# Performance work log

Hardware: AMD Instinct MI355X
Metric: run time of the kernel (lower is better)

The kernel has to match this reference:

```python
import jax, jax.numpy as jnp
import numpy as np

H = 128; D_T = 512; D_C = 256
NT = 20000; NC = 100000
E_TC = 100000; E_SIM = 800000; E_TS = 640000
K_APPNP = 10; ALPHA = 0.2


def setup_inputs() -> dict:
    key = jax.random.key(0)
    ki = iter(jax.random.split(key, 64))
    def nrm(shape, scale=1.0):
        return jax.random.normal(next(ki), shape, jnp.float32) * scale
    inp = {
        'table_x': nrm((NT, D_T)),
        'column_x': nrm((NC, D_C)),
        'q': nrm((D_T,)),
    }
    # layer-1 SAGEConv params per edge type: (src_dim, dst_dim)
    dims1 = {'tc': (D_T, D_C), 'rev': (D_C, D_T), 'cs': (D_C, D_C),
             'ns': (D_C, D_C), 'ds': (D_C, D_C), 'ts': (D_T, D_T)}
    for et, (dsrc, ddst) in dims1.items():
        inp['Wl1_' + et] = nrm((dsrc, H), 1.0 / np.sqrt(dsrc))
        inp['bl1_' + et] = jnp.zeros((H,), jnp.float32)
        inp['Wr1_' + et] = nrm((ddst, H), 1.0 / np.sqrt(ddst))
    # layer-2: only the convs that feed the 'table' output are needed
    for et in ('rev', 'ts'):
        inp['Wl2_' + et] = nrm((H, H), 1.0 / np.sqrt(H))
        inp['bl2_' + et] = jnp.zeros((H,), jnp.float32)
        inp['Wr2_' + et] = nrm((H, H), 1.0 / np.sqrt(H))
    inp['Wq'] = nrm((D_T, H), 1.0 / np.sqrt(D_T))
    inp['bq'] = jnp.zeros((H,), jnp.float32)
    inp['Wlin'] = nrm((H, 1), 1.0 / np.sqrt(H))
    inp['blin'] = jnp.zeros((1,), jnp.float32)
    inp['ts_ew'] = jax.random.uniform(next(ki), (E_TS,), jnp.float32)
    inp['tc_src'] = jax.random.randint(next(ki), (E_TC,), 0, NT)
    inp['tc_dst'] = jax.random.randint(next(ki), (E_TC,), 0, NC)
    inp['cs_ei'] = jax.random.randint(next(ki), (2, E_SIM), 0, NC)
    inp['ns_ei'] = jax.random.randint(next(ki), (2, E_SIM), 0, NC)
    inp['ds_ei'] = jax.random.randint(next(ki), (2, E_SIM), 0, NC)
    inp['ts_ei'] = jax.random.randint(next(ki), (2, E_TS), 0, NT)
    return inp


def _sage(xs, xd, src, dst, Wl, bl, Wr, n_dst):
    # PyG SAGEConv: lin_l(mean_{j in N(i)} x_j) + lin_r(x_i).
    # Linear commutes with mean, so project src features first (cheap gather).
    m = (xs @ Wl)[src]                                     # [E, H]
    s = jax.ops.segment_sum(m, dst, num_segments=n_dst)    # [n_dst, H]
    c = jax.ops.segment_sum(jnp.ones(src.shape, m.dtype), dst, num_segments=n_dst)
    return s / jnp.maximum(c, 1.0)[:, None] + bl + xd @ Wr


def _appnp(x, src, dst, ew, n):
    # gcn_norm with self-loops (fill value 1), then K personalized-PageRank steps
    loop = jnp.arange(n)
    s2 = jnp.concatenate([src, loop])
    d2 = jnp.concatenate([dst, loop])
    w2 = jnp.concatenate([ew, jnp.ones((n,), x.dtype)])
    deg = jax.ops.segment_sum(w2, d2, num_segments=n)
    dis = jnp.where(deg > 0, 1.0 / jnp.sqrt(deg), 0.0)
    norm = dis[s2] * w2 * dis[d2]                           # [E+n]
    def step(z, _):
        h = jax.ops.segment_sum(norm[:, None] * z[s2], d2, num_segments=n)
        return (1.0 - ALPHA) * h + ALPHA * x, None
    z, _ = jax.lax.scan(step, x, None, length=K_APPNP)
    return z


def reference(table_x, column_x, q, Wl1_tc, bl1_tc, Wr1_tc, Wl1_rev, bl1_rev, Wr1_rev,
              Wl1_cs, bl1_cs, Wr1_cs, Wl1_ns, bl1_ns, Wr1_ns, Wl1_ds, bl1_ds, Wr1_ds,
              Wl1_ts, bl1_ts, Wr1_ts, Wl2_rev, bl2_rev, Wr2_rev, Wl2_ts, bl2_ts, Wr2_ts,
              Wq, bq, Wlin, blin, ts_ew, tc_src, tc_dst, cs_ei, ns_ei, ds_ei, ts_ei):
    nT, nC = table_x.shape[0], column_x.shape[0]
    # ---- HeteroConv layer 1 (sum over edge types per destination type) ----
    col1 = (_sage(table_x, column_x, tc_src, tc_dst, Wl1_tc, bl1_tc, Wr1_tc, nC)
            + _sage(column_x, column_x, cs_ei[0], cs_ei[1], Wl1_cs, bl1_cs, Wr1_cs, nC)
            + _sage(column_x, column_x, ns_ei[0], ns_ei[1], Wl1_ns, bl1_ns, Wr1_ns, nC)
            + _sage(column_x, column_x, ds_ei[0], ds_ei[1], Wl1_ds, bl1_ds, Wr1_ds, nC))
    tab1 = (_sage(column_x, table_x, tc_dst, tc_src, Wl1_rev, bl1_rev, Wr1_rev, nT)
            + _sage(table_x, table_x, ts_ei[0], ts_ei[1], Wl1_ts, bl1_ts, Wr1_ts, nT))
    col1 = jax.nn.relu(col1)
    tab1 = jax.nn.relu(tab1)
    # ---- HeteroConv layer 2 (only the 'table' output is consumed) ----
    tab2 = (_sage(col1, tab1, tc_dst, tc_src, Wl2_rev, bl2_rev, Wr2_rev, nT)
            + _sage(tab1, tab1, ts_ei[0], ts_ei[1], Wl2_ts, bl2_ts, Wr2_ts, nT))
    # ---- retrieval-weighted query injection ----
    qv = q @ Wq + bq                                        # [H]
    eps = 1e-12
    xr = table_x / jnp.maximum(jnp.linalg.norm(table_x, axis=1, keepdims=True), eps)
    qr = q / jnp.maximum(jnp.linalg.norm(q), eps)
    wgt = jnp.maximum(xr @ qr, 0.0)                         # [nT]
    z0 = wgt[:, None] * qv[None, :]                         # [nT, H]
    # ---- APPNP diffusion over the table-sim graph ----
    z = _appnp(tab2 + z0, ts_ei[0], ts_ei[1], ts_ew, nT)
    return (z @ Wlin + blin)[:, 0]
```

## Files before the change

kernel.cpp:

```cpp
#include <hip/hip_runtime.h>

#define NT 20000
#define NC 100000
#define DT 512
#define DC 256
#define E_TC 100000
#define E_SIM 800000
#define E_TS 640000

#define KB_COL 0
#define KB_TAB (4 * NC)
#define NKEY   (4 * NC + 2 * NT)
#define NED_AB (3 * E_SIM + E_TC + E_TC + E_TS)
#define COLSTR 112
#define TABSTR 96
#define NPASS  4

typedef float f32x4 __attribute__((ext_vector_type(4)));
typedef __bf16 bf16x8 __attribute__((ext_vector_type(8)));


struct WD { const float* w0; const float* w1; const float* w2; const float* w3;
            __bf16* out; int K; int kshift; int ebase; };
struct WD8 { WD d[8]; };

__global__ void wprep_all(WD8 ds, int total) {
    int i = blockIdx.x * blockDim.x + threadIdx.x;
    if (i >= total) return;
#pragma unroll
    for (int s = 7; s >= 0; --s) {
        if (i >= ds.d[s].ebase) {
            const WD d = ds.d[s];
            const int idx = i - d.ebase;
            const int n = idx >> d.kshift;
            const int k = idx & (d.K - 1);
            float v = d.w0[(size_t)k * 128 + n];
            if (d.w1) v += d.w1[(size_t)k * 128 + n];
            if (d.w2) v += d.w2[(size_t)k * 128 + n];
            if (d.w3) v += d.w3[(size_t)k * 128 + n];
            d.out[(size_t)n * d.K + k] = (__bf16)v;
            return;
        }
    }
}

__global__ void vecprep(const float* __restrict__ q, const float* __restrict__ Wq,
                        const float* __restrict__ bq,
                        const float* __restrict__ Wr2_rev, const float* __restrict__ Wr2_ts,
                        const float* __restrict__ Wl2_rev, const float* __restrict__ Wl2_ts,
// ... 10 lines not shown
    biasT1[t] = bl1_rev[t] + bl1_ts[t];
    float a = 0.f, b = 0.f, c = 0.f;
    for (int h = 0; h < 128; ++h) {
        const float wl = Wlin[h];
        a = fmaf(Wr2_rev[(size_t)t * 128 + h] + Wr2_ts[(size_t)t * 128 + h], wl, a);
        b = fmaf(Wl2_rev[(size_t)t * 128 + h], wl, b);
        c = fmaf(Wl2_ts[(size_t)t * 128 + h], wl, c);
    }
    w2s[t] = a; wrev[t] = b; wts[t] = c;
    float qv = bq[t];
    for (int k = 0; k < 512; ++k) qv = fmaf(q[k], Wq[(size_t)k * 128 + t], qv);
    __shared__ float sh[128];
    sh[t] = qv * Wlin[t];
    __syncthreads();
    for (int st = 64; st >= 1; st >>= 1) { if (t < st) sh[t] += sh[t + st]; __syncthreads(); }
    if (t == 0) sc[0] = sh[0];
    __syncthreads();
    sh[t] = (bl2_rev[t] + bl2_ts[t]) * Wlin[t];
    __syncthreads();
    for (int st = 64; st >= 1; st >>= 1) { if (t < st) sh[t] += sh[t + st]; __syncthreads(); }
    if (t == 0) sc[1] = sh[0];
    __syncthreads();
    float ss = 0.f;
    for (int k = t; k < 512; k += 128) { const float v = q[k]; ss = fmaf(v, v, ss); }
    sh[t] = ss;
    __syncthreads();
    for (int st = 64; st >= 1; st >>= 1) { if (t < st) sh[t] += sh[t + st]; __syncthreads(); }
    if (t == 0) sc[2] = fmaxf(sqrtf(sh[0]), 1e-12f);
}


struct B5 { const __bf16* p[5]; };
struct Y5 { __bf16* p[5]; };

__launch_bounds__(256, 2)
__global__ void gemm_col5(const float* __restrict__ X, B5 wp, const float* __restrict__ bias,
                          Y5 yp, int M) {
    __shared__ __bf16 Bs[128 * 256];
    const int t = threadIdx.x;
    const int lane = t & 63;
    const int wave = t >> 6;
    const int l15 = lane & 15;
    const int kg = lane >> 4;
    const int rowbase = blockIdx.x * 128 + wave * 32;

    bf16x8 af[2][8];
#pragma unroll
    for (int m = 0; m < 2; ++m) {
        int r = rowbase + m * 16 + l15;
        r = (r < M) ? r : (M - 1);
        const float* baseA = X + (size_t)r * 256 + kg * 8;
#pragma unroll
        for (int ks = 0; ks < 8; ++ks) {
            const float4 x0 = *reinterpret_cast<const float4*>(baseA + ks * 32);
            const float4 x1 = *reinterpret_cast<const float4*>(baseA + ks * 32 + 4);
            bf16x8 tt;
            tt[0] = (__bf16)x0.x; tt[1] = (__bf16)x0.y; tt[2] = (__bf16)x0.z; tt[3] = (__bf16)x0.w;
            tt[4] = (__bf16)x1.x; tt[5] = (__bf16)x1.y; tt[6] = (__bf16)x1.z; tt[7] = (__bf16)x1.w;
            af[m][ks] = tt;
        }
    }

#pragma unroll
    for (int o = 0; o < 5; ++o) {
        __syncthreads();
        const __bf16* Wt = wp.p[o];
#pragma unroll
        for (int i = 0; i < 16; ++i) {
            const int u = t + i * 256;
            const int row = u >> 5;
            const int ku = u & 31;
            const bf16x8 v = *reinterpret_cast<const bf16x8*>(Wt + (size_t)row * 256 + ku * 8);
            *reinterpret_cast<bf16x8*>(&Bs[row * 256 + ((ku ^ (row & 7)) << 3)]) = v;
        }
        __syncthreads();
        f32x4 acc[2][8];
#pragma unroll
        for (int m = 0; m < 2; ++m)
#pragma unroll
            for (int n = 0; n < 8; ++n) acc[m][n] = (f32x4)0.f;
#pragma unroll
        for (int ks = 0; ks < 8; ++ks) {
            const int ku = ks * 4 + kg;
#pragma unroll
            for (int n = 0; n < 8; ++n) {
                const int r = n * 16 + l15;
                const bf16x8 bf = *reinterpret_cast<const bf16x8*>(&Bs[r * 256 + ((ku ^ (r & 7)) << 3)]);
                acc[0][n] = __builtin_amdgcn_mfma_f32_16x16x32_bf16(af[0][ks], bf, acc[0][n], 0, 0, 0);
                acc[1][n] = __builtin_amdgcn_mfma_f32_16x16x32_bf16(af[1][ks], bf, acc[1][n], 0, 0, 0);
            }
        }
        __bf16* Y = yp.p[o];
#pragma unroll
        for (int n = 0; n < 8; ++n) {
            const int col = n * 16 + l15;
            const float bv = (o == 0) ? bias[col] : 0.f;
#pragma unroll
            for (int m = 0; m < 2; ++m)
#pragma unroll
                for (int rr = 0; rr < 4; ++rr) {
                    const int row = rowbase + m * 16 + kg * 4 + rr;
                    if (row < M) Y[(size_t)row * 128 + col] = (__bf16)(acc[m][n][rr] + bv);
                }
        }
    }
}

struct B3 { const __bf16* p[3]; };
struct Y3 { __bf16* p[3]; };

__launch_bounds__(256, 2)
__global__ void gemm_tab3(const float* __restrict__ X, B3 wp, const float* __restrict__ bias,
                          Y3 yp, const float* __restrict__ q, const float* __restrict__ sc,
                          float* __restrict__ wgt, int M) {
    __shared__ __bf16 Bs[128 * 256];
    const int t = threadIdx.x;
    const int lane = t & 63;
    const int wave = t >> 6;
    const int l15 = lane & 15;
    const int kg = lane >> 4;
    const int rowbase = blockIdx.x * 64 + wave * 16;
    const int r0 = rowbase + l15;
    const bool rv = r0 < M;
    const int rc = rv ? r0 : (M - 1);
    const float* baseA = X + (size_t)rc * 512 + kg * 8;

    bf16x8 af[16];
    float dot = 0.f, ss = 0.f;
#pragma unroll
    for (int ks = 0; ks < 16; ++ks) {
        const float4 x0 = *reinterpret_cast<const float4*>(baseA + ks * 32);
        const float4 x1 = *reinterpret_cast<const float4*>(baseA + ks * 32 + 4);
        const float4 q0 = *reinterpret_cast<const float4*>(q + kg * 8 + ks * 32);
        const float4 q1 = *reinterpret_cast<const float4*>(q + kg * 8 + ks * 32 + 4);
        dot += x0.x * q0.x + x0.y * q0.y + x0.z * q0.z + x0.w * q0.w
             + x1.x * q1.x + x1.y * q1.y + x1.z * q1.z + x1.w * q1.w;
        ss += x0.x * x0.x + x0.y * x0.y + x0.z * x0.z + x0.w * x0.w
            + x1.x * x1.x + x1.y * x1.y + x1.z * x1.z + x1.w * x1.w;
        bf16x8 tt;
        tt[0] = (__bf16)x0.x; tt[1] = (__bf16)x0.y; tt[2] = (__bf16)x0.z; tt[3] = (__bf16)x0.w;
        tt[4] = (__bf16)x1.x; tt[5] = (__bf16)x1.y; tt[6] = (__bf16)x1.z; tt[7] = (__bf16)x1.w;
        af[ks] = tt;
    }
    dot += __shfl_xor(dot, 16); dot += __shfl_xor(dot, 32);
    ss  += __shfl_xor(ss, 16);  ss  += __shfl_xor(ss, 32);
    if (lane < 16 && rv) {
        const float nx = fmaxf(sqrtf(ss), 1e-12f);
        wgt[r0] = fmaxf(dot, 0.f) / (nx * sc[2]);
    }

#pragma unroll
    for (int o = 0; o < 3; ++o) {
        f32x4 acc[8];
#pragma unroll
        for (int n = 0; n < 8; ++n) acc[n] = (f32x4)0.f;
        const __bf16* Wt = wp.p[o];
#pragma unroll
        for (int c = 0; c < 2; ++c) {
            __syncthreads();
#pragma unroll
            for (int i = 0; i < 16; ++i) {
                const int u = t + i * 256;
                const int row = u >> 5;
                const int ku = u & 31;
                const bf16x8 v = *reinterpret_cast<const bf16x8*>(Wt + (size_t)row * 512 + c * 256 + ku * 8);
                *reinterpret_cast<bf16x8*>(&Bs[row * 256 + ((ku ^ (row & 7)) << 3)]) = v;
            }
            __syncthreads();
#pragma unroll
            for (int ks = 0; ks < 8; ++ks) {
                const int ku = ks * 4 + kg;
#pragma unroll
                for (int n = 0; n < 8; ++n) {
                    const int r = n * 16 + l15;
                    const bf16x8 bf = *reinterpret_cast<const bf16x8*>(&Bs[r * 256 + ((ku ^ (r & 7)) << 3)]);
                    acc[n] = __builtin_amdgcn_mfma_f32_16x16x32_bf16(af[c * 8 + ks], bf, acc[n], 0, 0, 0);
                }
            }
        }
        __bf16* Y = yp.p[o];
#pragma unroll
        for (int n = 0; n < 8; ++n) {
            const int col = n * 16 + l15;
            const float bv = (o == 0) ? bias[col] : 0.f;
#pragma unroll
            for (int rr = 0; rr < 4; ++rr) {
                const int row = rowbase + kg * 4 + rr;
                if (row < M) Y[(size_t)row * 128 + col] = (__bf16)(acc[n][rr] + bv);
            }
        }
    }
}


struct ED { const int* dst; const int* src; int E; int ebase; int ng; int g;
            int keybase; int srcoff; int ts; };
struct ED6 { ED d[6]; };

__global__ void fill_win(ED6 ds, const float* __restrict__ ew_ts,
                         const float* __restrict__ dis, int* __restrict__ cur,
                         int* __restrict__ ed_idx, int2* __restrict__ edT,
                         int lo, int hi, int total) {
    int e = blockIdx.x * blockDim.x + threadIdx.x;
    if (e >= total) return;
#pragma unroll
    for (int i = 5; i >= 0; --i) {
        if (e >= ds.d[i].ebase) {
            const ED d = ds.d[i];
            const int le = e - d.ebase;
            const int dstv = d.dst[le];
            const int key = d.keybase + dstv * d.ng + d.g;
            if (key >= lo && key < hi) {
                const int srcv = d.src[le];
                const int slot = atomicAdd(&cur[key], 1);
                if (key < KB_TAB) {
                    const int g = key & 3;
                    const int cap = (g < 3) ? 32 : 16;
                    if (slot < cap)
                        ed_idx[(key >> 2) * COLSTR + g * 32 + slot] = d.srcoff + srcv;
                } else {
                    const int k2 = key - KB_TAB;
                    const int g = k2 & 1;
                    const int cap = g ? 72 : 24;
                    if (slot < cap) {
                        int2 v;
                        v.x = d.srcoff + srcv;
                        v.y = d.ts ? __float_as_int(dis[srcv] * ew_ts[le] * dis[dstv]) : 0;
                        edT[(k2 >> 1) * TABSTR + g * 24 + slot] = v;
                    }
                }
            }
            return;
        }
    }
}

__global__ void deg_accum(const int* __restrict__ dst, const float* __restrict__ ew,
                          float* __restrict__ deg, int E) {
    int e = blockIdx.x * blockDim.x + threadIdx.x;
    if (e < E) atomicAdd(&deg[dst[e]], ew[e]);
}

__global__ void deg_to_dis(float* __restrict__ deg, int n) {
    int i = blockIdx.x * blockDim.x + threadIdx.x;
    if (i < n) {
        float d = deg[i];
        deg[i] = (d > 0.f) ? (1.0f / sqrtf(d)) : 0.f;
    }
}

__global__ void fill_f32(float* __restrict__ p, float v, int n) {
    int i = blockIdx.x * blockDim.x + threadIdx.x;
    if (i < n) p[i] = v;
}


__launch_bounds__(256)
__global__ void col_fused(const __bf16* __restrict__ selfRow, const __bf16* __restrict__ featCat,
                          const int* __restrict__ cur, const int* __restrict__ ed_idx,
                          const float* __restrict__ wvec, float* __restrict__ outv, int n) {
    const int wave = threadIdx.x >> 6;
    const int lane = threadIdx.x & 63;
    const int sg = lane >> 4;
    const int sl = lane & 15;
    const int row = blockIdx.x * 4 + wave;
    if (row >= n) return;
    const int4 l4 = *reinterpret_cast<const int4*>(&cur[row * 4]);
    int len[4];
    len[0] = (l4.x < 32) ? l4.x : 32;
    len[1] = (l4.y < 32) ? l4.y : 32;
    len[2] = (l4.z < 32) ? l4.z : 32;
    len[3] = (l4.w < 16) ? l4.w : 16;
    const int rowbase = row * COLSTR;
    float s8[8] = {0.f, 0.f, 0.f, 0.f, 0.f, 0.f, 0.f, 0.f};
#pragma unroll
    for (int g = 0; g < 4; ++g) {
        const int lg = len[g];
        if (lg <= 0) continue;
        const int base = rowbase + g * 32;
        const float w = 1.0f / (float)lg;
        int j = sg;
        for (; j + 4 < lg; j += 8) {
            const int s0 = ed_idx[base + j];
            const int s1 = ed_idx[base + j + 4];
            const bf16x8 v0 = *reinterpret_cast<const bf16x8*>(&featCat[(size_t)s0 * 128 + sl * 8]);
            const bf16x8 v1 = *reinterpret_cast<const bf16x8*>(&featCat[(size_t)s1 * 128 + sl * 8]);
// ... 65 lines not shown
        if (j < lg) {
            const int s0 = edT[base + j].x;
            const bf16x8 v0 = *reinterpret_cast<const bf16x8*>(&featCat[(size_t)s0 * 128 + sl * 8]);
#pragma unroll
            for (int t = 0; t < 8; ++t) s8[t] = fmaf(w, (float)v0[t], s8[t]);
        }
    }
#pragma unroll
    for (int t = 0; t < 8; ++t) {
        s8[t] += __shfl_xor(s8[t], 16);
        s8[t] += __shfl_xor(s8[t], 32);
    }
    const bf16x8 gv = *reinterpret_cast<const bf16x8*>(&selfRow[(size_t)row * 128 + sl * 8]);
    const float4 a0 = *reinterpret_cast<const float4*>(&wa[sl * 8]);
    const float4 a1 = *reinterpret_cast<const float4*>(&wa[sl * 8 + 4]);
    const float4 b0 = *reinterpret_cast<const float4*>(&wb[sl * 8]);
    const float4 b1 = *reinterpret_cast<const float4*>(&wb[sl * 8 + 4]);
    const float wwa[8] = {a0.x, a0.y, a0.z, a0.w, a1.x, a1.y, a1.z, a1.w};
    const float wwb[8] = {b0.x, b0.y, b0.z, b0.w, b1.x, b1.y, b1.z, b1.w};
    float da = 0.f, db = 0.f;
#pragma unroll
    for (int t = 0; t < 8; ++t) {
        const float rv = fmaxf(s8[t] + (float)gv[t], 0.f);
        da = fmaf(rv, wwa[t], da);
        db = fmaf(rv, wwb[t], db);
    }
#pragma unroll
    for (int off = 8; off; off >>= 1) { da += __shfl_xor(da, off); db += __shfl_xor(db, off); }
    if (lane == 0) { ya[row] = da; yb[row] = db; }
}


__launch_bounds__(256)
__global__ void y0_joint(const float* __restrict__ tvs, const float* __restrict__ val2,
                         const int* __restrict__ cur, const int2* __restrict__ edT,
                         const float* __restrict__ wgt, const float* __restrict__ sc,
                         float* __restrict__ y0, int n) {
    const int row = blockIdx.x * 16 + (threadIdx.x >> 4);
    const int l = threadIdx.x & 15;
    if (row >= n) return;
    const int2 l2 = *reinterpret_cast<const int2*>(&cur[KB_TAB + row * 2]);
    int len[2];
    len[0] = (l2.x < 24) ? l2.x : 24;
    len[1] = (l2.y < 72) ? l2.y : 72;
    const int rowbase = row * TABSTR;
    float s = 0.f;
#pragma unroll
    for (int g = 0; g < 2; ++g) {
        const int lg = len[g];
        if (lg <= 0) continue;
        const int base = rowbase + g * 24;
        const float w = 1.0f / (float)lg;
        for (int j = l; j < lg; j += 16)
            s = fmaf(w, val2[edT[base + j].x], s);
    }
#pragma unroll
    for (int off = 8; off; off >>= 1) s += __shfl_xor(s, off);
    if (l == 0) y0[row] = tvs[row] + sc[1] + wgt[row] * sc[0] + s;
}

__launch_bounds__(256)
__global__ void appnp_s(const float* __restrict__ z, const float* __restrict__ y0,
                        const int* __restrict__ cur, const int2* __restrict__ edT,
                        const float* __restrict__ dis, float* __restrict__ zo,
                        const float* __restrict__ blin, float* __restrict__ out,
                        int n, int last) {
    const int row = blockIdx.x * 16 + (threadIdx.x >> 4);
    const int l = threadIdx.x & 15;
    if (row >= n) return;
    int lg = cur[KB_TAB + row * 2 + 1];
    lg = (lg < 72) ? lg : 72;
    const int base = row * TABSTR + 24;
    float s = 0.f;
    int j = l;
    for (; j + 16 < lg; j += 32) {
        const int2 p0 = edT[base + j];
        const int2 p1 = edT[base + j + 16];
        s = fmaf(__int_as_float(p0.y), z[p0.x - NC], s);
        s = fmaf(__int_as_float(p1.y), z[p1.x - NC], s);
    }
    if (j < lg) {
        const int2 p0 = edT[base + j];
        s = fmaf(__int_as_float(p0.y), z[p0.x - NC], s);
    }
#pragma unroll
    for (int off = 8; off; off >>= 1) s += __shfl_xor(s, off);
    if (l == 0) {
        const float d = dis[row];
        const float v = 0.8f * (s + d * d * z[row]) + 0.2f * y0[row];
        if (last) out[row] = v + blin[0];
        else zo[row] = v;
    }
}


extern "C" void kernel_launch(void* const* d_in, const int* in_sizes, int n_in,
                              void* d_out, int out_size, void* d_ws, size_t ws_size,
                              hipStream_t stream) {
    const float* table_x  = (const float*)d_in[0];
    const float* column_x = (const float*)d_in[1];
    const float* q        = (const float*)d_in[2];
    const float* Wl1_tc  = (const float*)d_in[3];  const float* bl1_tc  = (const float*)d_in[4];  const float* Wr1_tc  = (const float*)d_in[5];
    const float* Wl1_rev = (const float*)d_in[6];  const float* bl1_rev = (const float*)d_in[7];  const float* Wr1_rev = (const float*)d_in[8];
    const float* Wl1_cs  = (const float*)d_in[9];  const float* bl1_cs  = (const float*)d_in[10]; const float* Wr1_cs  = (const float*)d_in[11];
    const float* Wl1_ns  = (const float*)d_in[12]; const float* bl1_ns  = (const float*)d_in[13]; const float* Wr1_ns  = (const float*)d_in[14];
    const float* Wl1_ds  = (const float*)d_in[15]; const float* bl1_ds  = (const float*)d_in[16]; const float* Wr1_ds  = (const float*)d_in[17];
    const float* Wl1_ts  = (const float*)d_in[18]; const float* bl1_ts  = (const float*)d_in[19]; const float* Wr1_ts  = (const float*)d_in[20];
    const float* Wl2_rev = (const float*)d_in[21]; const float* bl2_rev = (const float*)d_in[22]; const float* Wr2_rev = (const float*)d_in[23];
    const float* Wl2_ts  = (const float*)d_in[24]; const float* bl2_ts  = (const float*)d_in[25]; const float* Wr2_ts  = (const float*)d_in[26];
    const float* Wq   = (const float*)d_in[27]; const float* bq   = (const float*)d_in[28];
    const float* Wlin = (const float*)d_in[29]; const float* blin = (const float*)d_in[30];
    const float* ts_ew = (const float*)d_in[31];
    const int* tc_src = (const int*)d_in[32];
    const int* tc_dst = (const int*)d_in[33];
    const int* cs_ei  = (const int*)d_in[34];
    const int* ns_ei  = (const int*)d_in[35];
    const int* ds_ei  = (const int*)d_in[36];
    const int* ts_ei  = (const int*)d_in[37];

    char* w = (char*)d_ws;
    size_t off = 0;
    auto alloc = [&](size_t bytes) -> void* {
        void* p = w + off;
        off += (bytes + 255) & ~(size_t)255;
// ... 32 lines not shown
    float* f_wrev = (float*)alloc(128 * 4);
    float* f_wts  = (float*)alloc(128 * 4);
    float* f_sc   = (float*)alloc(16 * 4);
    int* i_cur  = (int*)alloc((size_t)NKEY * 4);
    int* ed_idx = (int*)alloc((size_t)NC * COLSTR * 4);
    int2* edT   = (int2*)alloc((size_t)NT * TABSTR * 8);
    if (off > ws_size) return;

    auto cdiv = [](int a, int b) { return (a + b - 1) / b; };

    {
        WD8 ds;
        int eb = 0;
        auto set = [&](int i, const float* a, const float* b2, const float* c, const float* d2,
                       __bf16* o, int K, int ksh) {
            ds.d[i] = {a, b2, c, d2, o, K, ksh, eb};
            eb += 128 * K;
        };
        set(0, Wr1_tc, Wr1_cs, Wr1_ns, Wr1_ds, WtS1c, 256, 8);
        set(1, Wl1_cs, nullptr, nullptr, nullptr, Wt_cs, 256, 8);
        set(2, Wl1_ns, nullptr, nullptr, nullptr, Wt_ns, 256, 8);
        set(3, Wl1_ds, nullptr, nullptr, nullptr, Wt_ds, 256, 8);
        set(4, Wl1_rev, nullptr, nullptr, nullptr, Wt_rev, 256, 8);
        set(5, Wl1_tc, nullptr, nullptr, nullptr, Wt_tc, 512, 9);
        set(6, Wr1_rev, Wr1_ts, nullptr, nullptr, WtS1t, 512, 9);
        set(7, Wl1_ts, nullptr, nullptr, nullptr, Wt_ts, 512, 9);
        wprep_all<<<cdiv(eb, 256), 256, 0, stream>>>(ds, eb);
    }
    vecprep<<<1, 128, 0, stream>>>(q, Wq, bq, Wr2_rev, Wr2_ts, Wl2_rev, Wl2_ts,
                                   bl2_rev, bl2_ts, Wlin, bl1_tc, bl1_cs, bl1_ns, bl1_ds,
                                   bl1_rev, bl1_ts, f_biasC, f_biasT1,
                                   f_w2s, f_wrev, f_wts, f_sc);

    {
        B5 wp; wp.p[0] = WtS1c; wp.p[1] = Wt_cs; wp.p[2] = Wt_ns; wp.p[3] = Wt_ds; wp.p[4] = Wt_rev;
        Y5 yp; yp.p[0] = gemmC; yp.p[1] = projC_cs; yp.p[2] = projC_ns; yp.p[3] = projC_ds; yp.p[4] = projC_rev;
        gemm_col5<<<cdiv(NC, 128), 256, 0, stream>>>(column_x, wp, f_biasC, yp, NC);
    }
    {
        B3 wp; wp.p[0] = WtS1t; wp.p[1] = Wt_tc; wp.p[2] = Wt_ts;
        Y3 yp; yp.p[0] = gemmT; yp.p[1] = projT_tc; yp.p[2] = projT_ts;
        gemm_tab3<<<cdiv(NT, 64), 256, 0, stream>>>(table_x, wp, f_biasT1, yp, q, f_sc, f_wgt, NT);
    }

    ED6 cds;
    cds.d[0] = {cs_ei + E_SIM, cs_ei, E_SIM, 0,                  4, 0, KB_COL, 0,      0};
    cds.d[1] = {ns_ei + E_SIM, ns_ei, E_SIM, E_SIM,              4, 1, KB_COL, NC,     0};
    cds.d[2] = {ds_ei + E_SIM, ds_ei, E_SIM, 2 * E_SIM,          4, 2, KB_COL, 2 * NC, 0};
    cds.d[3] = {tc_dst, tc_src, E_TC, 3 * E_SIM,                 4, 3, KB_COL, 3 * NC, 0};
    cds.d[4] = {tc_src, tc_dst, E_TC, 3 * E_SIM + E_TC,          2, 0, KB_TAB, 0,      0};
    cds.d[5] = {ts_ei + E_TS, ts_ei, E_TS, 3 * E_SIM + 2 * E_TC, 2, 1, KB_TAB, NC,     1};

    fill_f32<<<cdiv(NT, 256), 256, 0, stream>>>(f_dis, 1.0f, NT);
    deg_accum<<<cdiv(E_TS, 256), 256, 0, stream>>>(ts_ei + E_TS, ts_ew, f_dis, E_TS);
    deg_to_dis<<<cdiv(NT, 256), 256, 0, stream>>>(f_dis, NT);
    hipMemsetAsync(i_cur, 0, (size_t)NKEY * 4, stream);
    for (int p = 0; p < NPASS; ++p) {
        const int lo = (int)((long long)NKEY * p / NPASS);
        const int hi = (int)((long long)NKEY * (p + 1) / NPASS);
        fill_win<<<cdiv(NED_AB, 256), 256, 0, stream>>>(cds, ts_ew, f_dis, i_cur,
                                                        ed_idx, edT, lo, hi, NED_AB);
    }

    col_fused<<<cdiv(NC, 4), 256, 0, stream>>>(gemmC, featC, i_cur, ed_idx,
                                               f_wrev, f_colv, NC);
    tab_fused<<<cdiv(NT, 4), 256, 0, stream>>>(gemmT, featT, i_cur, edT,
                                               f_w2s, f_wts, f_tvs, f_tvt, NT);

    y0_joint<<<cdiv(NT, 16), 256, 0, stream>>>(f_tvs, val2, i_cur, edT,
                                               f_wgt, f_sc, f_y0, NT);

    const float* zin = f_y0;
    float* zout = f_za;
    for (int it = 0; it < 10; ++it) {
        const int last = (it == 9);
        appnp_s<<<cdiv(NT, 16), 256, 0, stream>>>(zin, f_y0, i_cur, edT,
                                                  f_dis, zout, blin, (float*)d_out, NT, last);
        zin = zout;
        zout = (zout == f_za) ? f_zb : f_za;
    }
}
```

Baseline: 587.4 us.

## Fuse GEMMs and edge bucketing into one heterogeneous kernel, defer edge normalization

```diff
diff --git a/kernel.cpp b/kernel.cpp
--- a/kernel.cpp
+++ b/kernel.cpp
@@ -14,7 +14,10 @@
 #define NED_AB (3 * E_SIM + E_TC + E_TC + E_TS)
 #define COLSTR 112
 #define TABSTR 96
-#define NPASS  4
+#define GCOL 782
+#define GTAB 313
+#define NFILL 365
+#define GRID_MEGA (GCOL + GTAB + NFILL)
 
 typedef float f32x4 __attribute__((ext_vector_type(4)));
 typedef __bf16 bf16x8 __attribute__((ext_vector_type(8)));
@@ -91,141 +94,103 @@
 
 struct B5 { const __bf16* p[5]; };
 struct Y5 { __bf16* p[5]; };
+struct B3 { const __bf16* p[3]; };
+struct Y3 { __bf16* p[3]; };
+struct ED { const int* dst; const int* src; int E; int ebase; int ng; int g;
+            int keybase; int srcoff; int ts; };
+struct ED6 { ED d[6]; };
 
 __launch_bounds__(256, 2)
-__global__ void gemm_col5(const float* __restrict__ X, B5 wp, const float* __restrict__ bias,
-                          Y5 yp, int M) {
+__global__ void mega(const float* __restrict__ Xc, B5 wpc, const float* __restrict__ biasC,
+                     Y5 ypc, const float* __restrict__ Xt, B3 wpt,
+                     const float* __restrict__ biasT, Y3 ypt,
+                     const float* __restrict__ q, const float* __restrict__ sc,
+                     float* __restrict__ wgt, ED6 cds, const float* __restrict__ ew_ts,
+                     float* __restrict__ deg, int* __restrict__ cur,
+                     int* __restrict__ ed_idx, int2* __restrict__ edT) {
     __shared__ __bf16 Bs[128 * 256];
+    const int bb = blockIdx.x;
+    const int bt = bb & 3;
     const int t = threadIdx.x;
+
+    if (bt == 3) {
+        for (int e = (bb >> 2) * 256 + t; e < NED_AB; e += NFILL * 256) {
+#pragma unroll
+            for (int i = 5; i >= 0; --i) {
+                if (e >= cds.d[i].ebase) {
+                    const ED d = cds.d[i];
+                    const int le = e - d.ebase;
+                    const int dstv = d.dst[le];
+                    const int key = d.keybase + dstv * d.ng + d.g;
+                    const int srcv = d.src[le];
+                    const int slot = atomicAdd(&cur[key], 1);
+                    if (key < KB_TAB) {
+                        const int g = key & 3;
+                        const int cap = (g < 3) ? 32 : 16;
+                        if (slot < cap)
+                            ed_idx[(key >> 2) * COLSTR + g * 32 + slot] = d.srcoff + srcv;
+                    } else {
+                        const int k2 = key - KB_TAB;
+                        if (k2 & 1) {
+                            const float ew = ew_ts[le];
+                            atomicAdd(&deg[dstv], ew);
+                            if (slot < 72)
+                                edT[(k2 >> 1) * TABSTR + 24 + slot] =
+                                    make_int2(NC + srcv, __float_as_int(ew));
+                        } else {
+                            if (slot < 24)
+                                edT[(k2 >> 1) * TABSTR + slot] = make_int2(srcv, 0);
+                        }
+                    }
+                    break;
+                }
+            }
+        }
+        return;
+    }
+
+    const int gi = (bb >> 2) * 3 + bt;
     const int lane = t & 63;
     const int wave = t >> 6;
     const int l15 = lane & 15;
     const int kg = lane >> 4;
-    const int rowbase = blockIdx.x * 128 + wave * 32;
-
-    bf16x8 af[2][8];
-#pragma unroll
-    for (int m = 0; m < 2; ++m) {
-        int r = rowbase + m * 16 + l15;
-        r = (r < M) ? r : (M - 1);
-        const float* baseA = X + (size_t)r * 256 + kg * 8;
-#pragma unroll
-        for (int ks = 0; ks < 8; ++ks) {
-            const float4 x0 = *reinterpret_cast<const float4*>(baseA + ks * 32);
-            const float4 x1 = *reinterpret_cast<const float4*>(baseA + ks * 32 + 4);
-            bf16x8 tt;
-            tt[0] = (__bf16)x0.x; tt[1] = (__bf16)x0.y; tt[2] = (__bf16)x0.z; tt[3] = (__bf16)x0.w;
-            tt[4] = (__bf16)x1.x; tt[5] = (__bf16)x1.y; tt[6] = (__bf16)x1.z; tt[7] = (__bf16)x1.w;
-            af[m][ks] = tt;
-        }
-    }
-
-#pragma unroll
-    for (int o = 0; o < 5; ++o) {
-        __syncthreads();
-        const __bf16* Wt = wp.p[o];
-#pragma unroll
-        for (int i = 0; i < 16; ++i) {
-            const int u = t + i * 256;
-            const int row = u >> 5;
-            const int ku = u & 31;
-            const bf16x8 v = *reinterpret_cast<const bf16x8*>(Wt + (size_t)row * 256 + ku * 8);
-            *reinterpret_cast<bf16x8*>(&Bs[row * 256 + ((ku ^ (row & 7)) << 3)]) = v;
-        }
-        __syncthreads();
-        f32x4 acc[2][8];
-#pragma unroll
-        for (int m = 0; m < 2; ++m)
-#pragma unroll
-            for (int n = 0; n < 8; ++n) acc[m][n] = (f32x4)0.f;
-#pragma unroll
-        for (int ks = 0; ks < 8; ++ks) {
-            const int ku = ks * 4 + kg;
-#pragma unroll
-            for (int n = 0; n < 8; ++n) {
-                const int r = n * 16 + l15;
-                const bf16x8 bf = *reinterpret_cast<const bf16x8*>(&Bs[r * 256 + ((ku ^ (r & 7)) << 3)]);
-                acc[0][n] = __builtin_amdgcn_mfma_f32_16x16x32_bf16(af[0][ks], bf, acc[0][n], 0, 0, 0);
-                acc[1][n] = __builtin_amdgcn_mfma_f32_16x16x32_bf16(af[1][ks], bf, acc[1][n], 0, 0, 0);
-            }
-        }
-        __bf16* Y = yp.p[o];
-#pragma unroll
-        for (int n = 0; n < 8; ++n) {
-            const int col = n * 16 + l15;
-            const float bv = (o == 0) ? bias[col] : 0.f;
-#pragma unroll
-            for (int m = 0; m < 2; ++m)
-#pragma unroll
-                for (int rr = 0; rr < 4; ++rr) {
-                    const int row = rowbase + m * 16 + kg * 4 + rr;
-                    if (row < M) Y[(size_t)row * 128 + col] = (__bf16)(acc[m][n][rr] + bv);
-                }
-        }
-    }
-}
-
-struct B3 { const __bf16* p[3]; };
-struct Y3 { __bf16* p[3]; };
-
-__launch_bounds__(256, 2)
-__global__ void gemm_tab3(const float* __restrict__ X, B3 wp, const float* __restrict__ bias,
-                          Y3 yp, const float* __restrict__ q, const float* __restrict__ sc,
-                          float* __restrict__ wgt, int M) {
-    __shared__ __bf16 Bs[128 * 256];
-    const int t = threadIdx.x;
-    const int lane = t & 63;
-    const int wave = t >> 6;
-    const int l15 = lane & 15;
-    const int kg = lane >> 4;
-    const int rowbase = blockIdx.x * 64 + wave * 16;
-    const int r0 = rowbase + l15;
-    const bool rv = r0 < M;
-    const int rc = rv ? r0 : (M - 1);
-    const float* baseA = X + (size_t)rc * 512 + kg * 8;
-
-    bf16x8 af[16];
-    float dot = 0.f, ss = 0.f;
-#pragma unroll
-    for (int ks = 0; ks < 16; ++ks) {
-        const float4 x0 = *reinterpret_cast<const float4*>(baseA + ks * 32);
-        const float4 x1 = *reinterpret_cast<const float4*>(baseA + ks * 32 + 4);
-        const float4 q0 = *reinterpret_cast<const float4*>(q + kg * 8 + ks * 32);
-        const float4 q1 = *reinterpret_cast<const float4*>(q + kg * 8 + ks * 32 + 4);
-        dot += x0.x * q0.x + x0.y * q0.y + x0.z * q0.z + x0.w * q0.w
-             + x1.x * q1.x + x1.y * q1.y + x1.z * q1.z + x1.w * q1.w;
-        ss += x0.x * x0.x + x0.y * x0.y + x0.z * x0.z + x0.w * x0.w
-            + x1.x * x1.x + x1.y * x1.y + x1.z * x1.z + x1.w * x1.w;
-        bf16x8 tt;
-        tt[0] = (__bf16)x0.x; tt[1] = (__bf16)x0.y; tt[2] = (__bf16)x0.z; tt[3] = (__bf16)x0.w;
-        tt[4] = (__bf16)x1.x; tt[5] = (__bf16)x1.y; tt[6] = (__bf16)x1.z; tt[7] = (__bf16)x1.w;
-        af[ks] = tt;
-    }
-    dot += __shfl_xor(dot, 16); dot += __shfl_xor(dot, 32);
-    ss  += __shfl_xor(ss, 16);  ss  += __shfl_xor(ss, 32);
-    if (lane < 16 && rv) {
-        const float nx = fmaxf(sqrtf(ss), 1e-12f);
-        wgt[r0] = fmaxf(dot, 0.f) / (nx * sc[2]);
-    }
-
-#pragma unroll
-    for (int o = 0; o < 3; ++o) {
-        f32x4 acc[8];
-#pragma unroll
-        for (int n = 0; n < 8; ++n) acc[n] = (f32x4)0.f;
-        const __bf16* Wt = wp.p[o];
-#pragma unroll
-        for (int c = 0; c < 2; ++c) {
+
+    if (gi < GCOL) {
+        const int rowbase = gi * 128 + wave * 32;
+        bf16x8 af[2][8];
+#pragma unroll
+        for (int m = 0; m < 2; ++m) {
+            int r = rowbase + m * 16 + l15;
+            r = (r < NC) ? r : (NC - 1);
+            const float* baseA = Xc + (size_t)r * 256 + kg * 8;
+#pragma unroll
+            for (int ks = 0; ks < 8; ++ks) {
+                const float4 x0 = *reinterpret_cast<const float4*>(baseA + ks * 32);
+                const float4 x1 = *reinterpret_cast<const float4*>(baseA + ks * 32 + 4);
+                bf16x8 tt;
+                tt[0] = (__bf16)x0.x; tt[1] = (__bf16)x0.y; tt[2] = (__bf16)x0.z; tt[3] = (__bf16)x0.w;
+                tt[4] = (__bf16)x1.x; tt[5] = (__bf16)x1.y; tt[6] = (__bf16)x1.z; tt[7] = (__bf16)x1.w;
+                af[m][ks] = tt;
+            }
+        }
+#pragma unroll
+        for (int o = 0; o < 5; ++o) {
             __syncthreads();
+            const __bf16* Wt = wpc.p[o];
 #pragma unroll
             for (int i = 0; i < 16; ++i) {
                 const int u = t + i * 256;
                 const int row = u >> 5;
                 const int ku = u & 31;
-                const bf16x8 v = *reinterpret_cast<const bf16x8*>(Wt + (size_t)row * 512 + c * 256 + ku * 8);
+                const bf16x8 v = *reinterpret_cast<const bf16x8*>(Wt + (size_t)row * 256 + ku * 8);
                 *reinterpret_cast<bf16x8*>(&Bs[row * 256 + ((ku ^ (row & 7)) << 3)]) = v;
             }
             __syncthreads();
+            f32x4 acc[2][8];
+#pragma unroll
+            for (int m = 0; m < 2; ++m)
+#pragma unroll
+                for (int n = 0; n < 8; ++n) acc[m][n] = (f32x4)0.f;
 #pragma unroll
             for (int ks = 0; ks < 8; ++ks) {
                 const int ku = ks * 4 + kg;
@@ -233,72 +198,102 @@
                 for (int n = 0; n < 8; ++n) {
                     const int r = n * 16 + l15;
                     const bf16x8 bf = *reinterpret_cast<const bf16x8*>(&Bs[r * 256 + ((ku ^ (r & 7)) << 3)]);
-                    acc[n] = __builtin_amdgcn_mfma_f32_16x16x32_bf16(af[c * 8 + ks], bf, acc[n], 0, 0, 0);
+                    acc[0][n] = __builtin_amdgcn_mfma_f32_16x16x32_bf16(af[0][ks], bf, acc[0][n], 0, 0, 0);
+                    acc[1][n] = __builtin_amdgcn_mfma_f32_16x16x32_bf16(af[1][ks], bf, acc[1][n], 0, 0, 0);
                 }
             }
-        }
-        __bf16* Y = yp.p[o];
-#pragma unroll
-        for (int n = 0; n < 8; ++n) {
-            const int col = n * 16 + l15;
-            const float bv = (o == 0) ? bias[col] : 0.f;
-#pragma unroll
-            for (int rr = 0; rr < 4; ++rr) {
-                const int row = rowbase + kg * 4 + rr;
-                if (row < M) Y[(size_t)row * 128 + col] = (__bf16)(acc[n][rr] + bv);
-            }
-        }
-    }
-}
-
-
-struct ED { const int* dst; const int* src; int E; int ebase; int ng; int g;
-            int keybase; int srcoff; int ts; };
-struct ED6 { ED d[6]; };
-
-__global__ void fill_win(ED6 ds, const float* __restrict__ ew_ts,
-                         const float* __restrict__ dis, int* __restrict__ cur,
-                         int* __restrict__ ed_idx, int2* __restrict__ edT,
-                         int lo, int hi, int total) {
-    int e = blockIdx.x * blockDim.x + threadIdx.x;
-    if (e >= total) return;
-#pragma unroll
-    for (int i = 5; i >= 0; --i) {
-        if (e >= ds.d[i].ebase) {
-            const ED d = ds.d[i];
-            const int le = e - d.ebase;
-            const int dstv = d.dst[le];
-            const int key = d.keybase + dstv * d.ng + d.g;
-            if (key >= lo && key < hi) {
-                const int srcv = d.src[le];
-                const int slot = atomicAdd(&cur[key], 1);
-                if (key < KB_TAB) {
-                    const int g = key & 3;
-                    const int cap = (g < 3) ? 32 : 16;
-                    if (slot < cap)
-                        ed_idx[(key >> 2) * COLSTR + g * 32 + slot] = d.srcoff + srcv;
-                } else {
-                    const int k2 = key - KB_TAB;
-                    const int g = k2 & 1;
-                    const int cap = g ? 72 : 24;
-                    if (slot < cap) {
-                        int2 v;
-                        v.x = d.srcoff + srcv;
-                        v.y = d.ts ? __float_as_int(dis[srcv] * ew_ts[le] * dis[dstv]) : 0;
-                        edT[(k2 >> 1) * TABSTR + g * 24 + slot] = v;
+            __bf16* Y = ypc.p[o];
+#pragma unroll
+            for (int n = 0; n < 8; ++n) {
+                const int col = n * 16 + l15;
+                const float bv = (o == 0) ? biasC[col] : 0.f;
+#pragma unroll
+                for (int m = 0; m < 2; ++m)
+#pragma unroll
+                    for (int rr = 0; rr < 4; ++rr) {
+                        const int row = rowbase + m * 16 + kg * 4 + rr;
+                        if (row < NC) Y[(size_t)row * 128 + col] = (__bf16)(acc[m][n][rr] + bv);
+                    }
+            }
+        }
+        return;
+    }
+
+    {
+        const int gb = gi - GCOL;
+        const int rowbase = gb * 64 + wave * 16;
+        const int r0 = rowbase + l15;
+        const bool rv = r0 < NT;
+        const int rc = rv ? r0 : (NT - 1);
+        const float* baseA = Xt + (size_t)rc * 512 + kg * 8;
+
+        bf16x8 af[16];
+        float dot = 0.f, ss = 0.f;
+#pragma unroll
+        for (int ks = 0; ks < 16; ++ks) {
+            const float4 x0 = *reinterpret_cast<const float4*>(baseA + ks * 32);
+            const float4 x1 = *reinterpret_cast<const float4*>(baseA + ks * 32 + 4);
+            const float4 q0 = *reinterpret_cast<const float4*>(q + kg * 8 + ks * 32);
+            const float4 q1 = *reinterpret_cast<const float4*>(q + kg * 8 + ks * 32 + 4);
+            dot += x0.x * q0.x + x0.y * q0.y + x0.z * q0.z + x0.w * q0.w
+                 + x1.x * q1.x + x1.y * q1.y + x1.z * q1.z + x1.w * q1.w;
+            ss += x0.x * x0.x + x0.y * x0.y + x0.z * x0.z + x0.w * x0.w
+                + x1.x * x1.x + x1.y * x1.y + x1.z * x1.z + x1.w * x1.w;
+            bf16x8 tt;
+            tt[0] = (__bf16)x0.x; tt[1] = (__bf16)x0.y; tt[2] = (__bf16)x0.z; tt[3] = (__bf16)x0.w;
+            tt[4] = (__bf16)x1.x; tt[5] = (__bf16)x1.y; tt[6] = (__bf16)x1.z; tt[7] = (__bf16)x1.w;
+            af[ks] = tt;
+        }
+        dot += __shfl_xor(dot, 16); dot += __shfl_xor(dot, 32);
+        ss  += __shfl_xor(ss, 16);  ss  += __shfl_xor(ss, 32);
+        if (lane < 16 && rv) {
+            const float nx = fmaxf(sqrtf(ss), 1e-12f);
+            wgt[r0] = fmaxf(dot, 0.f) / (nx * sc[2]);
+        }
+#pragma unroll
+        for (int o = 0; o < 3; ++o) {
+            f32x4 acc[8];
+#pragma unroll
+            for (int n = 0; n < 8; ++n) acc[n] = (f32x4)0.f;
+            const __bf16* Wt = wpt.p[o];
+#pragma unroll
+            for (int c = 0; c < 2; ++c) {
+                __syncthreads();
+#pragma unroll
+                for (int i = 0; i < 16; ++i) {
+                    const int u = t + i * 256;
+                    const int row = u >> 5;
+                    const int ku = u & 31;
+                    const bf16x8 v = *reinterpret_cast<const bf16x8*>(Wt + (size_t)row * 512 + c * 256 + ku * 8);
+                    *reinterpret_cast<bf16x8*>(&Bs[row * 256 + ((ku ^ (row & 7)) << 3)]) = v;
+                }
+                __syncthreads();
+#pragma unroll
+                for (int ks = 0; ks < 8; ++ks) {
+                    const int ku = ks * 4 + kg;
+#pragma unroll
+                    for (int n = 0; n < 8; ++n) {
+                        const int r = n * 16 + l15;
+                        const bf16x8 bf = *reinterpret_cast<const bf16x8*>(&Bs[r * 256 + ((ku ^ (r & 7)) << 3)]);
+                        acc[n] = __builtin_amdgcn_mfma_f32_16x16x32_bf16(af[c * 8 + ks], bf, acc[n], 0, 0, 0);
                     }
                 }
             }
-            return;
-        }
-    }
-}
-
-__global__ void deg_accum(const int* __restrict__ dst, const float* __restrict__ ew,
-                          float* __restrict__ deg, int E) {
-    int e = blockIdx.x * blockDim.x + threadIdx.x;
-    if (e < E) atomicAdd(&deg[dst[e]], ew[e]);
-}
+            __bf16* Y = ypt.p[o];
+#pragma unroll
+            for (int n = 0; n < 8; ++n) {
+                const int col = n * 16 + l15;
+                const float bv = (o == 0) ? biasT[col] : 0.f;
+#pragma unroll
+                for (int rr = 0; rr < 4; ++rr) {
+                    const int row = rowbase + kg * 4 + rr;
+                    if (row < NT) Y[(size_t)row * 128 + col] = (__bf16)(acc[n][rr] + bv);
+                }
+            }
+        }
+    }
+}
+
 
 __global__ void deg_to_dis(float* __restrict__ deg, int n) {
     int i = blockIdx.x * blockDim.x + threadIdx.x;
@@ -311,6 +306,20 @@
 __global__ void fill_f32(float* __restrict__ p, float v, int n) {
     int i = blockIdx.x * blockDim.x + threadIdx.x;
     if (i < n) p[i] = v;
+}
+
+__global__ void nrm_pass(int2* __restrict__ edT, const int* __restrict__ cur,
+                         const float* __restrict__ dis) {
+    int i = blockIdx.x * blockDim.x + threadIdx.x;
+    if (i >= NT * 72) return;
+    const int row = i / 72;
+    const int s = i - row * 72;
+    int lg = cur[KB_TAB + row * 2 + 1];
+    lg = (lg < 72) ? lg : 72;
+    if (s >= lg) return;
+    const int2 v = edT[row * TABSTR + 24 + s];
+    const float nv = dis[v.x - NC] * __int_as_float(v.y) * dis[row];
+    edT[row * TABSTR + 24 + s].y = __float_as_int(nv);
 }
 
 
@@ -461,8 +470,11 @@
         if (lg <= 0) continue;
         const int base = rowbase + g * 24;
         const float w = 1.0f / (float)lg;
-        for (int j = l; j < lg; j += 16)
-            s = fmaf(w, val2[edT[base + j].x], s);
+        for (int j = l; j < lg; j += 16) {
+            int idx = edT[base + j].x;
+            if (g == 1) idx -= NC;
+            s = fmaf(w, val2[g == 1 ? (NC + idx) : idx], s);
+        }
     }
 #pragma unroll
     for (int off = 8; off; off >>= 1) s += __shfl_xor(s, off);
@@ -598,16 +610,8 @@
                                    bl1_rev, bl1_ts, f_biasC, f_biasT1,
                                    f_w2s, f_wrev, f_wts, f_sc);
 
-    {
-        B5 wp; wp.p[0] = WtS1c; wp.p[1] = Wt_cs; wp.p[2] = Wt_ns; wp.p[3] = Wt_ds; wp.p[4] = Wt_rev;
-        Y5 yp; yp.p[0] = gemmC; yp.p[1] = projC_cs; yp.p[2] = projC_ns; yp.p[3] = projC_ds; yp.p[4] = projC_rev;
-        gemm_col5<<<cdiv(NC, 128), 256, 0, stream>>>(column_x, wp, f_biasC, yp, NC);
-    }
-    {
-        B3 wp; wp.p[0] = WtS1t; wp.p[1] = Wt_tc; wp.p[2] = Wt_ts;
-        Y3 yp; yp.p[0] = gemmT; yp.p[1] = projT_tc; yp.p[2] = projT_ts;
-        gemm_tab3<<<cdiv(NT, 64), 256, 0, stream>>>(table_x, wp, f_biasT1, yp, q, f_sc, f_wgt, NT);
-    }
+    fill_f32<<<cdiv(NT, 256), 256, 0, stream>>>(f_dis, 1.0f, NT);
+    hipMemsetAsync(i_cur, 0, (size_t)NKEY * 4, stream);
 
     ED6 cds;
     cds.d[0] = {cs_ei + E_SIM, cs_ei, E_SIM, 0,                  4, 0, KB_COL, 0,      0};
@@ -617,16 +621,19 @@
     cds.d[4] = {tc_src, tc_dst, E_TC, 3 * E_SIM + E_TC,          2, 0, KB_TAB, 0,      0};
     cds.d[5] = {ts_ei + E_TS, ts_ei, E_TS, 3 * E_SIM + 2 * E_TC, 2, 1, KB_TAB, NC,     1};
 
-    fill_f32<<<cdiv(NT, 256), 256, 0, stream>>>(f_dis, 1.0f, NT);
-    deg_accum<<<cdiv(E_TS, 256), 256, 0, stream>>>(ts_ei + E_TS, ts_ew, f_dis, E_TS);
+    {
+        B5 wpc; wpc.p[0] = WtS1c; wpc.p[1] = Wt_cs; wpc.p[2] = Wt_ns; wpc.p[3] = Wt_ds; wpc.p[4] = Wt_rev;
+        Y5 ypc; ypc.p[0] = gemmC; ypc.p[1] = projC_cs; ypc.p[2] = projC_ns; ypc.p[3] = projC_ds; ypc.p[4] = projC_rev;
+        B3 wpt; wpt.p[0] = WtS1t; wpt.p[1] = Wt_tc; wpt.p[2] = Wt_ts;
+        Y3 ypt; ypt.p[0] = gemmT; ypt.p[1] = projT_tc; ypt.p[2] = projT_ts;
+        mega<<<GRID_MEGA, 256, 0, stream>>>(column_x, wpc, f_biasC, ypc,
+                                            table_x, wpt, f_biasT1, ypt,
+                                            q, f_sc, f_wgt, cds, ts_ew,
+                                            f_dis, i_cur, ed_idx, edT);
+    }
+
     deg_to_dis<<<cdiv(NT, 256), 256, 0, stream>>>(f_dis, NT);
-    hipMemsetAsync(i_cur, 0, (size_t)NKEY * 4, stream);
-    for (int p = 0; p < NPASS; ++p) {
-        const int lo = (int)((long long)NKEY * p / NPASS);
-        const int hi = (int)((long long)NKEY * (p + 1) / NPASS);
-        fill_win<<<cdiv(NED_AB, 256), 256, 0, stream>>>(cds, ts_ew, f_dis, i_cur,
-                                                        ed_idx, edT, lo, hi, NED_AB);
-    }
+    nrm_pass<<<cdiv(NT * 72, 256), 256, 0, stream>>>(edT, i_cur, f_dis);
 
     col_fused<<<cdiv(NC, 4), 256, 0, stream>>>(gemmC, featC, i_cur, ed_idx,
                                                f_wrev, f_colv, NC);
```

Result: no change. 579.5 us (-1.3%).

## Fuse degree normalization, y0 and APPNP iterations into one cooperative kernel

Applied to the files above, without the earlier changes.

```diff
diff --git a/kernel.cpp b/kernel.cpp
--- a/kernel.cpp
+++ b/kernel.cpp
@@ -1,4 +1,7 @@
 #include <hip/hip_runtime.h>
+#include <hip/hip_cooperative_groups.h>
+
+namespace cg = cooperative_groups;
 
 #define NT 20000
 #define NC 100000
@@ -15,6 +18,7 @@
 #define COLSTR 112
 #define TABSTR 96
 #define NPASS  4
+#define GFILL  2048
 
 typedef float f32x4 __attribute__((ext_vector_type(4)));
 typedef __bf16 bf16x8 __attribute__((ext_vector_type(8)));
@@ -256,61 +260,42 @@
             int keybase; int srcoff; int ts; };
 struct ED6 { ED d[6]; };
 
-__global__ void fill_win(ED6 ds, const float* __restrict__ ew_ts,
-                         const float* __restrict__ dis, int* __restrict__ cur,
+__global__ void fill_win(ED6 ds, const float* __restrict__ ew_ts, int* __restrict__ cur,
                          int* __restrict__ ed_idx, int2* __restrict__ edT,
                          int lo, int hi, int total) {
-    int e = blockIdx.x * blockDim.x + threadIdx.x;
-    if (e >= total) return;
-#pragma unroll
-    for (int i = 5; i >= 0; --i) {
-        if (e >= ds.d[i].ebase) {
-            const ED d = ds.d[i];
-            const int le = e - d.ebase;
-            const int dstv = d.dst[le];
-            const int key = d.keybase + dstv * d.ng + d.g;
-            if (key >= lo && key < hi) {
-                const int srcv = d.src[le];
-                const int slot = atomicAdd(&cur[key], 1);
-                if (key < KB_TAB) {
-                    const int g = key & 3;
-                    const int cap = (g < 3) ? 32 : 16;
-                    if (slot < cap)
-                        ed_idx[(key >> 2) * COLSTR + g * 32 + slot] = d.srcoff + srcv;
-                } else {
-                    const int k2 = key - KB_TAB;
-                    const int g = k2 & 1;
-                    const int cap = g ? 72 : 24;
-                    if (slot < cap) {
-                        int2 v;
-                        v.x = d.srcoff + srcv;
-                        v.y = d.ts ? __float_as_int(dis[srcv] * ew_ts[le] * dis[dstv]) : 0;
-                        edT[(k2 >> 1) * TABSTR + g * 24 + slot] = v;
+    for (int e = blockIdx.x * blockDim.x + threadIdx.x; e < total;
+         e += gridDim.x * blockDim.x) {
+#pragma unroll
+        for (int i = 5; i >= 0; --i) {
+            if (e >= ds.d[i].ebase) {
+                const ED d = ds.d[i];
+                const int le = e - d.ebase;
+                const int dstv = d.dst[le];
+                const int key = d.keybase + dstv * d.ng + d.g;
+                if (key >= lo && key < hi) {
+                    const int srcv = d.src[le];
+                    const int slot = atomicAdd(&cur[key], 1);
+                    if (key < KB_TAB) {
+                        const int g = key & 3;
+                        const int cap = (g < 3) ? 32 : 16;
+                        if (slot < cap)
+                            ed_idx[(key >> 2) * COLSTR + g * 32 + slot] = d.srcoff + srcv;
+                    } else {
+                        const int k2 = key - KB_TAB;
+                        if (k2 & 1) {
+                            if (slot < 72)
+                                edT[(k2 >> 1) * TABSTR + 24 + slot] =
+                                    make_int2(NC + srcv, __float_as_int(ew_ts[le]));
+                        } else {
+                            if (slot < 24)
+                                edT[(k2 >> 1) * TABSTR + slot] = make_int2(srcv, 0);
+                        }
                     }
                 }
-            }
-            return;
-        }
-    }
-}
-
-__global__ void deg_accum(const int* __restrict__ dst, const float* __restrict__ ew,
-                          float* __restrict__ deg, int E) {
-    int e = blockIdx.x * blockDim.x + threadIdx.x;
-    if (e < E) atomicAdd(&deg[dst[e]], ew[e]);
-}
-
-__global__ void deg_to_dis(float* __restrict__ deg, int n) {
-    int i = blockIdx.x * blockDim.x + threadIdx.x;
-    if (i < n) {
-        float d = deg[i];
-        deg[i] = (d > 0.f) ? (1.0f / sqrtf(d)) : 0.f;
-    }
-}
-
-__global__ void fill_f32(float* __restrict__ p, float v, int n) {
-    int i = blockIdx.x * blockDim.x + threadIdx.x;
-    if (i < n) p[i] = v;
+                break;
+            }
+        }
+    }
 }
 
 
@@ -442,64 +427,83 @@
 
 
 __launch_bounds__(256)
-__global__ void y0_joint(const float* __restrict__ tvs, const float* __restrict__ val2,
-                         const int* __restrict__ cur, const int2* __restrict__ edT,
-                         const float* __restrict__ wgt, const float* __restrict__ sc,
-                         float* __restrict__ y0, int n) {
+__global__ void tail_coop(const int* __restrict__ cur, int2* __restrict__ edT,
+                          const float* __restrict__ tvs, const float* __restrict__ val2,
+                          const float* __restrict__ wgt, const float* __restrict__ sc,
+                          const float* __restrict__ blin, float* __restrict__ dis,
+                          float* __restrict__ y0, float* __restrict__ za,
+                          float* __restrict__ zb, float* __restrict__ out) {
+    cg::grid_group grid = cg::this_grid();
     const int row = blockIdx.x * 16 + (threadIdx.x >> 4);
     const int l = threadIdx.x & 15;
-    if (row >= n) return;
-    const int2 l2 = *reinterpret_cast<const int2*>(&cur[KB_TAB + row * 2]);
-    int len[2];
-    len[0] = (l2.x < 24) ? l2.x : 24;
-    len[1] = (l2.y < 72) ? l2.y : 72;
-    const int rowbase = row * TABSTR;
-    float s = 0.f;
-#pragma unroll
-    for (int g = 0; g < 2; ++g) {
-        const int lg = len[g];
-        if (lg <= 0) continue;
-        const int base = rowbase + g * 24;
-        const float w = 1.0f / (float)lg;
-        for (int j = l; j < lg; j += 16)
-            s = fmaf(w, val2[edT[base + j].x], s);
-    }
-#pragma unroll
-    for (int off = 8; off; off >>= 1) s += __shfl_xor(s, off);
-    if (l == 0) y0[row] = tvs[row] + sc[1] + wgt[row] * sc[0] + s;
-}
-
-__launch_bounds__(256)
-__global__ void appnp_s(const float* __restrict__ z, const float* __restrict__ y0,
-                        const int* __restrict__ cur, const int2* __restrict__ edT,
-                        const float* __restrict__ dis, float* __restrict__ zo,
-                        const float* __restrict__ blin, float* __restrict__ out,
-                        int n, int last) {
-    const int row = blockIdx.x * 16 + (threadIdx.x >> 4);
-    const int l = threadIdx.x & 15;
-    if (row >= n) return;
-    int lg = cur[KB_TAB + row * 2 + 1];
-    lg = (lg < 72) ? lg : 72;
-    const int base = row * TABSTR + 24;
-    float s = 0.f;
-    int j = l;
-    for (; j + 16 < lg; j += 32) {
-        const int2 p0 = edT[base + j];
-        const int2 p1 = edT[base + j + 16];
-        s = fmaf(__int_as_float(p0.y), z[p0.x - NC], s);
-        s = fmaf(__int_as_float(p1.y), z[p1.x - NC], s);
-    }
-    if (j < lg) {
-        const int2 p0 = edT[base + j];
-        s = fmaf(__int_as_float(p0.y), z[p0.x - NC], s);
-    }
-#pragma unroll
-    for (int off = 8; off; off >>= 1) s += __shfl_xor(s, off);
-    if (l == 0) {
-        const float d = dis[row];
-        const float v = 0.8f * (s + d * d * z[row]) + 0.2f * y0[row];
-        if (last) out[row] = v + blin[0];
-        else zo[row] = v;
+    const bool ok = row < NT;
+    int lenR = 0, lenT = 0, baseR = 0, baseT = 0;
+    if (ok) {
+        const int2 l2 = *reinterpret_cast<const int2*>(&cur[KB_TAB + row * 2]);
+        lenR = (l2.x < 24) ? l2.x : 24;
+        lenT = (l2.y < 72) ? l2.y : 72;
+        baseR = row * TABSTR;
+        baseT = row * TABSTR + 24;
+    }
+    if (ok) {
+        float sdeg = 0.f, sy = 0.f;
+        const float wR = (lenR > 0) ? 1.0f / (float)lenR : 0.f;
+        for (int j = l; j < lenR; j += 16) sy = fmaf(wR, val2[edT[baseR + j].x], sy);
+        const float wT = (lenT > 0) ? 1.0f / (float)lenT : 0.f;
+        for (int j = l; j < lenT; j += 16) {
+            const int2 p = edT[baseT + j];
+            sdeg += __int_as_float(p.y);
+            sy = fmaf(wT, val2[p.x], sy);
+        }
+#pragma unroll
+        for (int off = 8; off; off >>= 1) {
+            sdeg += __shfl_xor(sdeg, off);
+            sy += __shfl_xor(sy, off);
+        }
+        if (l == 0) {
+            const float dg = sdeg + 1.0f;
+            dis[row] = (dg > 0.f) ? (1.0f / sqrtf(dg)) : 0.f;
+            y0[row] = tvs[row] + sc[1] + wgt[row] * sc[0] + sy;
+        }
+    }
+    grid.sync();
+    if (ok) {
+        const float dr = dis[row];
+        for (int j = l; j < lenT; j += 16) {
+            const int2 p = edT[baseT + j];
+            const float nv = dis[p.x - NC] * __int_as_float(p.y) * dr;
+            edT[baseT + j].y = __float_as_int(nv);
+        }
+    }
+    grid.sync();
+    const float* zin = y0;
+    float* zo = za;
+    for (int it = 0; it < 10; ++it) {
+        if (ok) {
+            float s = 0.f;
+            int j = l;
+            for (; j + 16 < lenT; j += 32) {
+                const int2 p0 = edT[baseT + j];
+                const int2 p1 = edT[baseT + j + 16];
+                s = fmaf(__int_as_float(p0.y), zin[p0.x - NC], s);
+                s = fmaf(__int_as_float(p1.y), zin[p1.x - NC], s);
+            }
+            if (j < lenT) {
+                const int2 p0 = edT[baseT + j];
+                s = fmaf(__int_as_float(p0.y), zin[p0.x - NC], s);
+            }
+#pragma unroll
+            for (int off = 8; off; off >>= 1) s += __shfl_xor(s, off);
+            if (l == 0) {
+                const float d = dis[row];
+                const float v = 0.8f * (s + d * d * zin[row]) + 0.2f * y0[row];
+                if (it == 9) out[row] = v + blin[0];
+                else zo[row] = v;
+            }
+        }
+        grid.sync();
+        zin = zo;
+        zo = (zo == za) ? zb : za;
     }
 }
 
@@ -617,15 +621,11 @@
     cds.d[4] = {tc_src, tc_dst, E_TC, 3 * E_SIM + E_TC,          2, 0, KB_TAB, 0,      0};
     cds.d[5] = {ts_ei + E_TS, ts_ei, E_TS, 3 * E_SIM + 2 * E_TC, 2, 1, KB_TAB, NC,     1};
 
-    fill_f32<<<cdiv(NT, 256), 256, 0, stream>>>(f_dis, 1.0f, NT);
-    deg_accum<<<cdiv(E_TS, 256), 256, 0, stream>>>(ts_ei + E_TS, ts_ew, f_dis, E_TS);
-    deg_to_dis<<<cdiv(NT, 256), 256, 0, stream>>>(f_dis, NT);
     hipMemsetAsync(i_cur, 0, (size_t)NKEY * 4, stream);
     for (int p = 0; p < NPASS; ++p) {
         const int lo = (int)((long long)NKEY * p / NPASS);
         const int hi = (int)((long long)NKEY * (p + 1) / NPASS);
-        fill_win<<<cdiv(NED_AB, 256), 256, 0, stream>>>(cds, ts_ew, f_dis, i_cur,
-                                                        ed_idx, edT, lo, hi, NED_AB);
+        fill_win<<<GFILL, 256, 0, stream>>>(cds, ts_ew, i_cur, ed_idx, edT, lo, hi, NED_AB);
     }
 
     col_fused<<<cdiv(NC, 4), 256, 0, stream>>>(gemmC, featC, i_cur, ed_idx,
@@ -633,16 +633,12 @@
     tab_fused<<<cdiv(NT, 4), 256, 0, stream>>>(gemmT, featT, i_cur, edT,
                                                f_w2s, f_wts, f_tvs, f_tvt, NT);
 
-    y0_joint<<<cdiv(NT, 16), 256, 0, stream>>>(f_tvs, val2, i_cur, edT,
-                                               f_wgt, f_sc, f_y0, NT);
-
-    const float* zin = f_y0;
-    float* zout = f_za;
-    for (int it = 0; it < 10; ++it) {
-        const int last = (it == 9);
-        appnp_s<<<cdiv(NT, 16), 256, 0, stream>>>(zin, f_y0, i_cur, edT,
-                                                  f_dis, zout, blin, (float*)d_out, NT, last);
-        zin = zout;
-        zout = (zout == f_za) ? f_zb : f_za;
-    }
-}
+    {
+        float* outp = (float*)d_out;
+        void* args[] = {(void*)&i_cur, (void*)&edT, (void*)&f_tvs, (void*)&val2,
+                        (void*)&f_wgt, (void*)&f_sc, (void*)&blin, (void*)&f_dis,
+                        (void*)&f_y0, (void*)&f_za, (void*)&f_zb, (void*)&outp};
+        hipLaunchCooperativeKernel((void*)tail_coop, dim3(cdiv(NT, 16)), dim3(256),
+                                   args, 0, stream);
+    }
+}
```

New measurement: 1.967 ms. 235% more time.
